# Kernel optimization log

Hardware: AMD Instinct MI355X
Metric: run time of the kernel (lower is better)

Reference implementation:

```python
import jax, jax.numpy as jnp
import numpy as np

# --- model dims (from init args) ---
LAYERS = 6
LEAF = 2 ** (LAYERS - 1)        # 32
M_LEN = 128
CAM_NUM = 2
MAIN_CAM = 0
LATENT = 48
H_LAT = 2048                    # LatentNet hidden
H_BR = 512                      # ChooseBranchNet hidden
B = 16384

# Path bits: for leaf i, bit at classifier depth d (root->leaf order) is
# (i >> (LAYERS-2-d)) & 1. This is exactly what the search_table + double
# advanced-indexing gather in the torch code computes (heap tree routing).
_BITS = ((np.arange(LEAF)[:, None] >> np.arange(LAYERS - 2, -1, -1)[None, :]) & 1)  # [LEAF, LAYERS-1]
BITS = jnp.asarray(_BITS, dtype=jnp.int32)


def setup_inputs() -> dict:
    key = jax.random.key(0)
    ks = jax.random.split(key, 9)
    s = lambda fan: 1.0 / np.sqrt(fan)
    return {
        "batch_data": jax.random.normal(ks[0], (B, CAM_NUM, M_LEN), dtype=jnp.float32),
        # LatentNet: [B, 2*M_LEN] -> hidden -> LEAF*LATENT
        "Wl1": jax.random.normal(ks[1], (2 * M_LEN, H_LAT), dtype=jnp.float32) * s(2 * M_LEN),
        "bl1": jnp.zeros((H_LAT,), dtype=jnp.float32),
        "Wl2": jax.random.normal(ks[2], (H_LAT, LEAF * LATENT), dtype=jnp.float32) * s(H_LAT),
        "bl2": jnp.zeros((LEAF * LATENT,), dtype=jnp.float32),
        # ChooseBranchNet (shared across the LAYERS-1 classifier slots): M_LEN -> hidden -> 2
        "Wb1": jax.random.normal(ks[3], (M_LEN, H_BR), dtype=jnp.float32) * s(M_LEN),
        "bb1": jnp.zeros((H_BR,), dtype=jnp.float32),
        "Wb2": jax.random.normal(ks[4], (H_BR, 2), dtype=jnp.float32) * s(H_BR),
        "bb2": jnp.zeros((2,), dtype=jnp.float32),
    }


def reference(batch_data, Wl1, bl1, Wl2, bl2, Wb1, bb1, Wb2, bb2):
    bsz = batch_data.shape[0]
    # expand_measurements: main cam repeated (LAYERS-1) times -> [B, LAYERS-1, M_LEN]
    main = batch_data[:, MAIN_CAM]                                  # [B, M_LEN]
    x_br = jnp.broadcast_to(main[:, None, :], (bsz, LAYERS - 1, M_LEN))
    # ChooseBranchNet -> per-layer 2-way probabilities
    h = jax.nn.relu(jnp.einsum('blm,mh->blh', x_br, Wb1) + bb1)
    p = jax.nn.softmax(jnp.einsum('blh,ho->blo', h, Wb2) + bb2, axis=-1)  # [B, L-1, 2]
    # Tree gates: product of path-branch probabilities along root->leaf path.
    comp = jnp.where(BITS[None] == 1, p[:, None, :, 1], p[:, None, :, 0])  # [B, LEAF, L-1]
    gates = jnp.prod(comp, axis=-1)                                        # [B, LEAF]
    # top-1 routing (argsort(...)[:, -1] as in the torch code)
    router = jnp.argsort(gates, axis=-1)[:, -1]                            # [B]
    # LatentNet on concatenated two-camera measurements
    x2 = jnp.concatenate([batch_data[:, 0], batch_data[:, 1]], axis=-1)    # [B, 2*M_LEN]
    hl = jax.nn.relu(x2 @ Wl1 + bl1)
    nn_latent = (hl @ Wl2 + bl2).reshape(bsz, LEAF, LATENT)
    # scatter-select per-sample leaf latent (replaces the torch.where loop)
    select = jnp.take_along_axis(nn_latent, router[:, None, None], axis=1)[:, 0]  # [B, LATENT]
    return select
```

## Files before the change

kernel.cpp:

```cpp
#include <hip/hip_runtime.h>
#include <stdint.h>

typedef short bf16x8 __attribute__((ext_vector_type(8)));
typedef float f32x4 __attribute__((ext_vector_type(4)));

#define NROWS 16384
#define K1DIM 256
#define N1DIM 2048
#define N2DIM 96
#define MARGIN 0.03f

#define GLD16(g, l) __builtin_amdgcn_global_load_lds( \
    (const __attribute__((address_space(1))) uint32_t*)(g), \
    (__attribute__((address_space(3))) uint32_t*)(l), 16, 0, 0)

__device__ __forceinline__ ushort f2bf(float x) {
  union { float f; uint32_t u; } c; c.f = x;
  uint32_t u = c.u;
  return (ushort)((u + 0x7FFFu + ((u >> 16) & 1u)) >> 16);
}

__global__ __launch_bounds__(256) void k0_convert(
    const float* __restrict__ bd, const float* __restrict__ Wl1,
    const float* __restrict__ Wl2, const float* __restrict__ Wb1,
    ushort* __restrict__ x2bf, ushort* __restrict__ wl1t,
    ushort* __restrict__ w2t, ushort* __restrict__ wb1t) {
  int i = blockIdx.x * 256 + threadIdx.x;
  if (i < NROWS * 256) x2bf[i] = f2bf(bd[i]);
  if (i < 2048 * 256) {
    int n = i >> 8, k = i & 255;
    wl1t[i] = f2bf(Wl1[k * 2048 + n]);
  }
  if (i < 96 * 2048) {
    int j = i >> 11, k = i & 2047;
    int col = (j < 48) ? j : (1440 + j);
    w2t[i] = f2bf(Wl2[k * 1536 + col]);
  }
  if (i < 512 * 128) {
    int j = i >> 7, m = i & 127;
    wb1t[i] = f2bf(Wb1[m * 512 + j]);
  }
}

__global__ __launch_bounds__(256) void k1a_score(
    const ushort* __restrict__ x2bf, const ushort* __restrict__ wb1t,
    const float* __restrict__ bb1, const float* __restrict__ Wb2,
    float* __restrict__ part) {
  __shared__ __align__(1024) ushort As[128 * 64];
  __shared__ __align__(1024) ushort Bs[128 * 64];
  const int t = threadIdx.x, ln = t & 63, wv = t >> 6;
  const int m0 = blockIdx.y << 7;
  const int n0 = blockIdx.x << 7;
  const int wm = (wv >> 1) << 6, wn = (wv & 1) << 6;
  const int rsub = ln >> 3, kc8 = ln & 7;
  const int q = ln >> 4, rr = ln & 15;

  f32x4 acc[4][4] = {};

  for (int k0 = 0; k0 < 128; k0 += 64) {
#pragma unroll
    for (int i = 0; i < 4; i++) {
      int inst = (wv << 2) + i;
      int row = (inst << 3) + rsub;
      GLD16(x2bf + (size_t)(m0 + row) * 256 + k0 + (kc8 << 3), As + (inst << 9));
      GLD16(wb1t + (size_t)(n0 + row) * 128 + k0 + (kc8 << 3), Bs + (inst << 9));
    }
    __syncthreads();
#pragma unroll
    for (int kk = 0; kk < 2; kk++) {
      int kb = ((kk << 2) + q) << 3;
      bf16x8 af[4], bfr[4];
#pragma unroll
      for (int mi = 0; mi < 4; mi++)
        af[mi] = *(const bf16x8*)(As + (((wm + (mi << 4) + rr)) << 6) + kb);
#pragma unroll
      for (int ni = 0; ni < 4; ni++)
        bfr[ni] = *(const bf16x8*)(Bs + (((wn + (ni << 4) + rr)) << 6) + kb);
#pragma unroll
      for (int mi = 0; mi < 4; mi++)
#pragma unroll
        for (int ni = 0; ni < 4; ni++)
          acc[mi][ni] = __builtin_amdgcn_mfma_f32_16x16x32_bf16(
              af[mi], bfr[ni], acc[mi][ni], 0, 0, 0);
    }
    __syncthreads();
  }

  float s4[4][4] = {};
#pragma unroll
  for (int ni = 0; ni < 4; ni++) {
    int col = n0 + wn + (ni << 4) + rr;
    float bias = bb1[col];
    float wdv = Wb2[col * 2 + 1] - Wb2[col * 2];
#pragma unroll
    for (int mi = 0; mi < 4; mi++) {
      f32x4 a = acc[mi][ni];
#pragma unroll
      for (int v = 0; v < 4; v++)
        s4[mi][v] += fmaxf(a[v] + bias, 0.f) * wdv;
    }
  }
#pragma unroll
  for (int off = 1; off <= 8; off <<= 1)
#pragma unroll
    for (int mi = 0; mi < 4; mi++)
#pragma unroll
      for (int v = 0; v < 4; v++)
        s4[mi][v] += __shfl_xor(s4[mi][v], off);

  if (rr == 0) {
    float* dst = part + (size_t)(blockIdx.x * 2 + (wv & 1)) * NROWS +
                 m0 + wm + (q << 2);
#pragma unroll
    for (int mi = 0; mi < 4; mi++) {
      float4 v4 = make_float4(s4[mi][0], s4[mi][1], s4[mi][2], s4[mi][3]);
      *(float4*)(dst + (mi << 4)) = v4;
    }
  }
}

__global__ __launch_bounds__(256) void k1b_classify(
    const float* __restrict__ part, const float* __restrict__ bb2,
    int* __restrict__ router, int* __restrict__ list, int* __restrict__ counter) {
  int t = blockIdx.x * 256 + threadIdx.x;
  float s = bb2[1] - bb2[0];
#pragma unroll
  for (int i = 0; i < 8; i++) s += part[i * NROWS + t];
  router[t] = (s >= 0.f) ? 1 : 0;
  if (fabsf(s) < MARGIN) {
    int idx = atomicAdd(counter, 1);
    list[idx] = t;
  }
}

__global__ __launch_bounds__(256) void k1c_recheck(
    const float* __restrict__ bd, const float* __restrict__ Wb1,
    const float* __restrict__ Wb2, const float* __restrict__ bb1,
    const float* __restrict__ bb2, const int* __restrict__ list,
    const int* __restrict__ counter, int* __restrict__ router) {
  const int ln = threadIdx.x & 63;
  const int wid = (blockIdx.x * 256 + threadIdx.x) >> 6;
  const int count = *counter;
  const float c = bb2[1] - bb2[0];

  for (int base = wid * 4; base < count; base += 512 * 4) {
    int rows[4];
#pragma unroll
    for (int r = 0; r < 4; r++) {
      int idx = base + r;
      rows[r] = list[(idx < count) ? idx : base];
    }
    float acc[4][8];
#pragma unroll
    for (int r = 0; r < 4; r++)
#pragma unroll
      for (int u = 0; u < 8; u++) acc[r][u] = 0.f;

    for (int m = 0; m < 128; m++) {
      float w[8];
#pragma unroll
      for (int u = 0; u < 8; u++) w[u] = Wb1[m * 512 + (u << 6) + ln];
#pragma unroll
      for (int r = 0; r < 4; r++) {
        float x = bd[(size_t)rows[r] * 256 + m];
#pragma unroll
        for (int u = 0; u < 8; u++) acc[r][u] = fmaf(x, w[u], acc[r][u]);
      }
    }
    float sc[4];
#pragma unroll
    for (int r = 0; r < 4; r++) {
      float s = 0.f;
#pragma unroll
      for (int u = 0; u < 8; u++) {
        int j = (u << 6) + ln;
        float wd = Wb2[j * 2 + 1] - Wb2[j * 2];
        s += fmaxf(acc[r][u] + bb1[j], 0.f) * wd;
      }
#pragma unroll
      for (int off = 1; off <= 32; off <<= 1) s += __shfl_xor(s, off);
      sc[r] = s + c;
    }
    if (ln == 0) {
#pragma unroll
      for (int r = 0; r < 4; r++)
        if (base + r < count) router[rows[r]] = (sc[r] >= 0.f) ? 1 : 0;
    }
  }
}

__global__ __launch_bounds__(256) void k2_gemm1(
    const ushort* __restrict__ A, const ushort* __restrict__ BT,
    const float* __restrict__ bl1, ushort* __restrict__ hl) {
  __shared__ __align__(1024) ushort As[128 * 64];
  __shared__ __align__(1024) ushort Bs[128 * 64];
  const int t = threadIdx.x, ln = t & 63, wv = t >> 6;
  const int m0 = blockIdx.y << 7;
  const int n0 = blockIdx.x << 7;
  const int wm = (wv >> 1) << 6, wn = (wv & 1) << 6;
  const int rsub = ln >> 3, kc8 = ln & 7;
  const int q = ln >> 4, rr = ln & 15;

  f32x4 acc[4][4] = {};

  for (int k0 = 0; k0 < K1DIM; k0 += 64) {
#pragma unroll
    for (int i = 0; i < 4; i++) {
      int inst = (wv << 2) + i;
      int row = (inst << 3) + rsub;
      GLD16(A + (size_t)(m0 + row) * K1DIM + k0 + (kc8 << 3), As + (inst << 9));
      GLD16(BT + (size_t)(n0 + row) * K1DIM + k0 + (kc8 << 3), Bs + (inst << 9));
    }
    __syncthreads();
#pragma unroll
    for (int kk = 0; kk < 2; kk++) {
      int kb = ((kk << 2) + q) << 3;
      bf16x8 af[4], bfr[4];
#pragma unroll
      for (int mi = 0; mi < 4; mi++)
        af[mi] = *(const bf16x8*)(As + (((wm + (mi << 4) + rr)) << 6) + kb);
#pragma unroll
      for (int ni = 0; ni < 4; ni++)
        bfr[ni] = *(const bf16x8*)(Bs + (((wn + (ni << 4) + rr)) << 6) + kb);
#pragma unroll
      for (int mi = 0; mi < 4; mi++)
#pragma unroll
        for (int ni = 0; ni < 4; ni++)
          acc[mi][ni] = __builtin_amdgcn_mfma_f32_16x16x32_bf16(
              af[mi], bfr[ni], acc[mi][ni], 0, 0, 0);
    }
    __syncthreads();
  }

#pragma unroll
  for (int ni = 0; ni < 4; ni++) {
    int col = n0 + wn + (ni << 4) + rr;
    float bias = bl1[col];
#pragma unroll
    for (int mi = 0; mi < 4; mi++) {
      int rowb = m0 + wm + (mi << 4) + (q << 2);
      f32x4 a = acc[mi][ni];
#pragma unroll
      for (int v = 0; v < 4; v++) {
        float val = fmaxf(a[v] + bias, 0.f);
        hl[(size_t)(rowb + v) * N1DIM + col] = f2bf(val);
      }
    }
  }
}

__global__ __launch_bounds__(256) void k2b_gemm2(
    const ushort* __restrict__ hl, const ushort* __restrict__ w2t,
    float* __restrict__ P) {
  __shared__ __align__(1024) ushort As[64 * 64];
  __shared__ __align__(1024) ushort Bs[96 * 64];
  const int t = threadIdx.x, ln = t & 63, wv = t >> 6;
  const int ks = blockIdx.x;
  const int rb = blockIdx.y << 6;
  const int rsub = ln >> 3, kc8 = ln & 7;
  const int q = ln >> 4, rr = ln & 15;
  float* Pout = P + (size_t)ks * NROWS * N2DIM;
  const int kbase = ks << 10;

  f32x4 acc[6] = {};

  for (int k0 = 0; k0 < 1024; k0 += 64) {
    int kg = kbase + k0;
#pragma unroll
    for (int i = 0; i < 2; i++) {
      int inst = (wv << 1) + i;
      int row = (inst << 3) + rsub;
      GLD16(hl + (size_t)(rb + row) * N1DIM + kg + (kc8 << 3), As + (inst << 9));
    }
#pragma unroll
    for (int i = 0; i < 3; i++) {
      int inst = wv * 3 + i;
      int row = (inst << 3) + rsub;
      GLD16(w2t + (size_t)row * N1DIM + kg + (kc8 << 3), Bs + (inst << 9));
    }
    __syncthreads();
#pragma unroll
    for (int kk = 0; kk < 2; kk++) {
      int kb = ((kk << 2) + q) << 3;
      bf16x8 af = *(const bf16x8*)(As + (((wv << 4) + rr) << 6) + kb);
#pragma unroll
      for (int ni = 0; ni < 6; ni++) {
        bf16x8 bfr = *(const bf16x8*)(Bs + (((ni << 4) + rr) << 6) + kb);
        acc[ni] = __builtin_amdgcn_mfma_f32_16x16x32_bf16(af, bfr, acc[ni], 0, 0, 0);
      }
    }
    __syncthreads();
  }

#pragma unroll
  for (int ni = 0; ni < 6; ni++) {
#pragma unroll
    for (int v = 0; v < 4; v++) {
      int row = rb + (wv << 4) + (q << 2) + v;
      int col = (ni << 4) + rr;
      Pout[(size_t)row * N2DIM + col] = acc[ni][v];
    }
  }
}

__global__ __launch_bounds__(256) void k3_select(
    const float* __restrict__ P0, const float* __restrict__ P1,
    const float* __restrict__ bl2, const int* __restrict__ router,
    float* __restrict__ out) {
  int t = blockIdx.x * 256 + threadIdx.x;
  int b = t / 12, i4 = (t % 12) * 4;
  int sel = router[b];
  int cb = sel ? 48 : 0;
  int bb = sel ? 1488 : 0;
  float4 p0 = *(const float4*)(P0 + (size_t)b * N2DIM + cb + i4);
  float4 p1 = *(const float4*)(P1 + (size_t)b * N2DIM + cb + i4);
  float4 bz = *(const float4*)(bl2 + bb + i4);
  float4 r;
  r.x = p0.x + p1.x + bz.x;
  r.y = p0.y + p1.y + bz.y;
  r.z = p0.z + p1.z + bz.z;
  r.w = p0.w + p1.w + bz.w;
  *(float4*)(out + (size_t)b * 48 + i4) = r;
}

extern "C" void kernel_launch(void* const* d_in, const int* in_sizes, int n_in,
                              void* d_out, int out_size, void* d_ws, size_t ws_size,
                              hipStream_t stream) {
  const float* bd  = (const float*)d_in[0];
  const float* Wl1 = (const float*)d_in[1];
  const float* bl1 = (const float*)d_in[2];
  const float* Wl2 = (const float*)d_in[3];
  const float* bl2 = (const float*)d_in[4];
  const float* Wb1 = (const float*)d_in[5];
  const float* bb1 = (const float*)d_in[6];
  const float* Wb2 = (const float*)d_in[7];
  const float* bb2 = (const float*)d_in[8];

  char* ws = (char*)d_ws;
  ushort* x2bf  = (ushort*)(ws);
  ushort* wl1t  = (ushort*)(ws + 8388608);
  ushort* w2t   = (ushort*)(ws + 9437184);
  ushort* hl    = (ushort*)(ws + 9830400);
  float*  P     = (float*)(ws + 76939264);
  int*    router= (int*)(ws + 89522176);
  ushort* wb1t  = (ushort*)(ws + 89587712);
  float*  part  = (float*)(ws + 89718784);
  int*    list  = (int*)(ws + 90243072);
  int*    counter=(int*)(ws + 90308608);
  float*  outp  = (float*)d_out;

  k0_convert<<<dim3(16384), dim3(256), 0, stream>>>(bd, Wl1, Wl2, Wb1,
                                                    x2bf, wl1t, w2t, wb1t);
  hipMemsetAsync(counter, 0, 4, stream);
  k1a_score<<<dim3(4, 128), dim3(256), 0, stream>>>(x2bf, wb1t, bb1, Wb2, part);
  k1b_classify<<<dim3(64), dim3(256), 0, stream>>>(part, bb2, router, list, counter);
  k1c_recheck<<<dim3(128), dim3(256), 0, stream>>>(bd, Wb1, Wb2, bb1, bb2,
                                                   list, counter, router);
  k2_gemm1<<<dim3(16, 128), dim3(256), 0, stream>>>(x2bf, wl1t, bl1, hl);
  k2b_gemm2<<<dim3(2, 256), dim3(256), 0, stream>>>(hl, w2t, P);
  k3_select<<<dim3(768), dim3(256), 0, stream>>>(P, P + (size_t)NROWS * N2DIM, bl2,
                                                 router, outp);
}
```

Measured before the change: 184.2 us.

## Fuse the two LatentNet GEMMs so the hidden activations stay in LDS

Merges the first GEMM (x2 @ Wl1 with bias and ReLU) and the second GEMM (hidden @ Wl2) into one kernel. Each block computes 128-column chunks of the hidden layer for 64 rows, stores them as bf16 in shared memory, and accumulates them straight into the split-K partial output. This removes the 64 MB bf16 hidden-activation write and re-read through global memory and drops one launch. In exchange the grid is only 512 blocks, each looping serially over 8 chunks, shared memory use per block grows, and the x2 tiles are reloaded for every chunk.

```diff
diff --git a/kernel.cpp b/kernel.cpp
--- a/kernel.cpp
+++ b/kernel.cpp
@@ -189,104 +189,97 @@
   }
 }
 
-__global__ __launch_bounds__(256) void k2_gemm1(
-    const ushort* __restrict__ A, const ushort* __restrict__ BT,
-    const float* __restrict__ bl1, ushort* __restrict__ hl) {
-  __shared__ __align__(1024) ushort As[128 * 64];
-  __shared__ __align__(1024) ushort Bs[128 * 64];
-  const int t = threadIdx.x, ln = t & 63, wv = t >> 6;
-  const int m0 = blockIdx.y << 7;
-  const int n0 = blockIdx.x << 7;
-  const int wm = (wv >> 1) << 6, wn = (wv & 1) << 6;
-  const int rsub = ln >> 3, kc8 = ln & 7;
-  const int q = ln >> 4, rr = ln & 15;
-
-  f32x4 acc[4][4] = {};
-
-  for (int k0 = 0; k0 < K1DIM; k0 += 64) {
-#pragma unroll
-    for (int i = 0; i < 4; i++) {
-      int inst = (wv << 2) + i;
-      int row = (inst << 3) + rsub;
-      GLD16(A + (size_t)(m0 + row) * K1DIM + k0 + (kc8 << 3), As + (inst << 9));
-      GLD16(BT + (size_t)(n0 + row) * K1DIM + k0 + (kc8 << 3), Bs + (inst << 9));
-    }
-    __syncthreads();
-#pragma unroll
-    for (int kk = 0; kk < 2; kk++) {
-      int kb = ((kk << 2) + q) << 3;
-      bf16x8 af[4], bfr[4];
-#pragma unroll
-      for (int mi = 0; mi < 4; mi++)
-        af[mi] = *(const bf16x8*)(As + (((wm + (mi << 4) + rr)) << 6) + kb);
-#pragma unroll
-      for (int ni = 0; ni < 4; ni++)
-        bfr[ni] = *(const bf16x8*)(Bs + (((wn + (ni << 4) + rr)) << 6) + kb);
-#pragma unroll
-      for (int mi = 0; mi < 4; mi++)
-#pragma unroll
-        for (int ni = 0; ni < 4; ni++)
-          acc[mi][ni] = __builtin_amdgcn_mfma_f32_16x16x32_bf16(
-              af[mi], bfr[ni], acc[mi][ni], 0, 0, 0);
-    }
-    __syncthreads();
-  }
-
-#pragma unroll
-  for (int ni = 0; ni < 4; ni++) {
-    int col = n0 + wn + (ni << 4) + rr;
-    float bias = bl1[col];
-#pragma unroll
-    for (int mi = 0; mi < 4; mi++) {
-      int rowb = m0 + wm + (mi << 4) + (q << 2);
-      f32x4 a = acc[mi][ni];
-#pragma unroll
-      for (int v = 0; v < 4; v++) {
-        float val = fmaxf(a[v] + bias, 0.f);
-        hl[(size_t)(rowb + v) * N1DIM + col] = f2bf(val);
-      }
-    }
-  }
-}
-
-__global__ __launch_bounds__(256) void k2b_gemm2(
-    const ushort* __restrict__ hl, const ushort* __restrict__ w2t,
+__global__ __launch_bounds__(256) void k2_fused(
+    const ushort* __restrict__ x2bf, const ushort* __restrict__ wl1t,
+    const ushort* __restrict__ w2t, const float* __restrict__ bl1,
     float* __restrict__ P) {
   __shared__ __align__(1024) ushort As[64 * 64];
-  __shared__ __align__(1024) ushort Bs[96 * 64];
+  __shared__ __align__(1024) ushort Bs[128 * 64];
+  __shared__ __align__(1024) ushort Ws[2 * 96 * 64];
+  __shared__ __align__(1024) ushort Hs[64 * 136];
   const int t = threadIdx.x, ln = t & 63, wv = t >> 6;
-  const int ks = blockIdx.x;
-  const int rb = blockIdx.y << 6;
+  const int ks2 = blockIdx.x;
+  const int m0 = blockIdx.y << 6;
+  const int q = ln >> 4, rr = ln & 15;
   const int rsub = ln >> 3, kc8 = ln & 7;
-  const int q = ln >> 4, rr = ln & 15;
-  float* Pout = P + (size_t)ks * NROWS * N2DIM;
-  const int kbase = ks << 10;
-
-  f32x4 acc[6] = {};
-
-  for (int k0 = 0; k0 < 1024; k0 += 64) {
-    int kg = kbase + k0;
-#pragma unroll
-    for (int i = 0; i < 2; i++) {
-      int inst = (wv << 1) + i;
-      int row = (inst << 3) + rsub;
-      GLD16(hl + (size_t)(rb + row) * N1DIM + kg + (kc8 << 3), As + (inst << 9));
-    }
-#pragma unroll
-    for (int i = 0; i < 3; i++) {
-      int inst = wv * 3 + i;
-      int row = (inst << 3) + rsub;
-      GLD16(w2t + (size_t)row * N1DIM + kg + (kc8 << 3), Bs + (inst << 9));
+
+  f32x4 accP[6] = {};
+
+  for (int nc = 0; nc < 8; nc++) {
+    const int n0 = (ks2 << 10) + (nc << 7);
+
+#pragma unroll
+    for (int j = 0; j < 6; j++) {
+      int inst = wv * 6 + j;
+      int h = inst / 12;
+      int r0 = (inst - h * 12) << 3;
+      GLD16(w2t + (size_t)(r0 + rsub) * 2048 + n0 + (h << 6) + (kc8 << 3),
+            Ws + h * 6144 + ((inst - h * 12) << 9));
+    }
+
+    f32x4 acc1[4][2] = {};
+    for (int k0 = 0; k0 < K1DIM; k0 += 64) {
+#pragma unroll
+      for (int i = 0; i < 2; i++) {
+        int inst = (wv << 1) + i;
+        int row = (inst << 3) + rsub;
+        GLD16(x2bf + (size_t)(m0 + row) * K1DIM + k0 + (kc8 << 3),
+              As + (inst << 9));
+      }
+#pragma unroll
+      for (int i = 0; i < 4; i++) {
+        int inst = (wv << 2) + i;
+        int row = (inst << 3) + rsub;
+        GLD16(wl1t + (size_t)(n0 + row) * K1DIM + k0 + (kc8 << 3),
+              Bs + (inst << 9));
+      }
+      __syncthreads();
+#pragma unroll
+      for (int kk = 0; kk < 2; kk++) {
+        int kb = (kk << 5) + (q << 3);
+        bf16x8 af[4], bfr[2];
+#pragma unroll
+        for (int mi = 0; mi < 4; mi++)
+          af[mi] = *(const bf16x8*)(As + (((mi << 4) + rr) << 6) + kb);
+#pragma unroll
+        for (int ni = 0; ni < 2; ni++)
+          bfr[ni] = *(const bf16x8*)(Bs + (((wv << 5) + (ni << 4) + rr) << 6) + kb);
+#pragma unroll
+        for (int mi = 0; mi < 4; mi++)
+#pragma unroll
+          for (int ni = 0; ni < 2; ni++)
+            acc1[mi][ni] = __builtin_amdgcn_mfma_f32_16x16x32_bf16(
+                af[mi], bfr[ni], acc1[mi][ni], 0, 0, 0);
+      }
+      __syncthreads();
+    }
+
+#pragma unroll
+    for (int ni = 0; ni < 2; ni++) {
+      int lcol = (wv << 5) + (ni << 4) + rr;
+      float bias = bl1[n0 + lcol];
+#pragma unroll
+      for (int mi = 0; mi < 4; mi++) {
+        f32x4 a = acc1[mi][ni];
+#pragma unroll
+        for (int v = 0; v < 4; v++) {
+          int lrow = (mi << 4) + (q << 2) + v;
+          Hs[lrow * 136 + lcol] = f2bf(fmaxf(a[v] + bias, 0.f));
+        }
+      }
     }
     __syncthreads();
-#pragma unroll
-    for (int kk = 0; kk < 2; kk++) {
-      int kb = ((kk << 2) + q) << 3;
-      bf16x8 af = *(const bf16x8*)(As + (((wv << 4) + rr) << 6) + kb);
+
+#pragma unroll
+    for (int kk = 0; kk < 4; kk++) {
+      int half = kk >> 1;
+      int k64 = (kk & 1) << 5;
+      bf16x8 ha = *(const bf16x8*)(Hs + ((wv << 4) + rr) * 136 + (kk << 5) + (q << 3));
 #pragma unroll
       for (int ni = 0; ni < 6; ni++) {
-        bf16x8 bfr = *(const bf16x8*)(Bs + (((ni << 4) + rr) << 6) + kb);
-        acc[ni] = __builtin_amdgcn_mfma_f32_16x16x32_bf16(af, bfr, acc[ni], 0, 0, 0);
+        bf16x8 wb = *(const bf16x8*)(Ws + half * 6144 +
+                                     (((ni << 4) + rr) << 6) + k64 + (q << 3));
+        accP[ni] = __builtin_amdgcn_mfma_f32_16x16x32_bf16(ha, wb, accP[ni], 0, 0, 0);
       }
     }
     __syncthreads();
@@ -296,9 +289,9 @@
   for (int ni = 0; ni < 6; ni++) {
 #pragma unroll
     for (int v = 0; v < 4; v++) {
-      int row = rb + (wv << 4) + (q << 2) + v;
+      int row = m0 + (wv << 4) + (q << 2) + v;
       int col = (ni << 4) + rr;
-      Pout[(size_t)row * N2DIM + col] = acc[ni][v];
+      P[(size_t)ks2 * NROWS * N2DIM + (size_t)row * N2DIM + col] = accP[ni][v];
     }
   }
 }
@@ -340,7 +333,6 @@
   ushort* x2bf  = (ushort*)(ws);
   ushort* wl1t  = (ushort*)(ws + 8388608);
   ushort* w2t   = (ushort*)(ws + 9437184);
-  ushort* hl    = (ushort*)(ws + 9830400);
   float*  P     = (float*)(ws + 76939264);
   int*    router= (int*)(ws + 89522176);
   ushort* wb1t  = (ushort*)(ws + 89587712);
@@ -356,8 +348,7 @@
   k1b_classify<<<dim3(64), dim3(256), 0, stream>>>(part, bb2, router, list, counter);
   k1c_recheck<<<dim3(128), dim3(256), 0, stream>>>(bd, Wb1, Wb2, bb1, bb2,
                                                    list, counter, router);
-  k2_gemm1<<<dim3(16, 128), dim3(256), 0, stream>>>(x2bf, wl1t, bl1, hl);
-  k2b_gemm2<<<dim3(2, 256), dim3(256), 0, stream>>>(hl, w2t, P);
+  k2_fused<<<dim3(2, 256), dim3(256), 0, stream>>>(x2bf, wl1t, w2t, bl1, P);
   k3_select<<<dim3(768), dim3(256), 0, stream>>>(P, P + (size_t)NROWS * N2DIM, bl2,
                                                  router, outp);
 }
```

New measurement: 186.5 us. Within noise of the previous version (+1.3%).
